# Optimization experiments

Hardware: AMD Instinct MI355X
Metric: run time of the kernel (lower is better)

## Reference

```python
import jax, jax.numpy as jnp
import numpy as np

N = 20000        # nodes
E = 320000       # edges (avg degree 16)
F_IN = 128       # node_features
F2 = 64          # second_features (per-head out dim, LSTM hidden)
H = 8            # heads
D1 = H * F2      # 512, concat output of GATConv / LSTM input
NEG_SLOPE = 0.2  # GATConv default leaky_relu slope


def _gat_conv(x, src, dst, W, att_src, att_dst, bias):
    """PyG GATConv (concat=True, self-loops added, eval-mode dropout)."""
    n = x.shape[0]
    h = (x @ W).reshape(n, H, -1)                      # [N,H,F]
    a_s = (h * att_src).sum(-1)                        # [N,H]
    a_d = (h * att_dst).sum(-1)                        # [N,H]
    e = jax.nn.leaky_relu(a_s[src] + a_d[dst], NEG_SLOPE)   # [E',H]
    m = jax.ops.segment_max(e, dst, num_segments=n)    # [N,H]
    m = jnp.where(jnp.isfinite(m), m, 0.0)
    ex = jnp.exp(e - m[dst])
    denom = jax.ops.segment_sum(ex, dst, num_segments=n)
    alpha = ex / (denom[dst] + 1e-16)                  # [E',H]
    msg = h[src] * alpha[:, :, None]                   # [E',H,F]
    out = jax.ops.segment_sum(msg, dst, num_segments=n)  # [N,H,F]
    return out.reshape(n, -1) + bias                   # [N,H*F]


def _lstm_step(x, W_ih, W_hh, b_ih, b_hh):
    """Single-timestep PyTorch LSTM with zero initial (h0, c0). x: [N,D1]."""
    h0 = jnp.zeros((x.shape[0], F2), x.dtype)
    gates = x @ W_ih.T + b_ih + h0 @ W_hh.T + b_hh     # [N,4*F2]
    i, f, g, o = jnp.split(gates, 4, axis=-1)
    c = jax.nn.sigmoid(f) * 0.0 + jax.nn.sigmoid(i) * jnp.tanh(g)
    h = jax.nn.sigmoid(o) * jnp.tanh(c)
    return h, (h, c)


def setup_inputs() -> dict:
    key = jax.random.key(0)
    ks = jax.random.split(key, 16)

    def glorot(k, shape, fan_in):
        return jax.random.normal(k, shape, jnp.float32) * (1.0 / np.sqrt(fan_in))

    return {
        "x": jax.random.normal(ks[0], (N, F_IN), jnp.float32),
        "edge_index": jax.random.randint(ks[1], (2, E), 0, N, jnp.int32),
        "edge_weight": jax.random.uniform(ks[2], (E,), jnp.float32),
        # GATConv 1: F_IN -> H*F2
        "W1": glorot(ks[3], (F_IN, H * F2), F_IN),
        "att_src1": glorot(ks[4], (H, F2), F2),
        "att_dst1": glorot(ks[5], (H, F2), F2),
        "bias1": jnp.zeros((H * F2,), jnp.float32),
        # LSTM: input D1 -> hidden F2
        "W_ih": glorot(ks[6], (4 * F2, D1), D1),
        "W_hh": glorot(ks[7], (4 * F2, F2), F2),
        "b_ih": jnp.zeros((4 * F2,), jnp.float32),
        "b_hh": jnp.zeros((4 * F2,), jnp.float32),
        # GATConv 2: F2 -> H*F2
        "W2": glorot(ks[8], (F2, H * F2), F2),
        "att_src2": glorot(ks[9], (H, F2), F2),
        "att_dst2": glorot(ks[10], (H, F2), F2),
        "bias2": jnp.zeros((H * F2,), jnp.float32),
    }


def reference(x, edge_index, edge_weight, W1, att_src1, att_dst1, bias1,
              W_ih, W_hh, b_ih, b_hh, W2, att_src2, att_dst2, bias2):
    # edge_weight is accepted but unused, matching the original forward.
    loops = jnp.arange(N, dtype=edge_index.dtype)
    src = jnp.concatenate([edge_index[0], loops])      # add self-loops (PyG default)
    dst = jnp.concatenate([edge_index[1], loops])

    h = _gat_conv(x, src, dst, W1, att_src1, att_dst1, bias1)   # [N,512]
    h, hidden2 = _lstm_step(h, W_ih, W_hh, b_ih, b_hh)          # [N,64]
    h = jax.nn.relu(h)
    h = _gat_conv(h, src, dst, W2, att_src2, att_dst2, bias2)   # [N,512]
    return jax.nn.softmax(h, axis=1)
```

## Files before the change

### kernel.cpp

```cpp
#include <hip/hip_runtime.h>
#include <math.h>


__global__ void count_kernel(const int* __restrict__ dst, int* __restrict__ deg, int E) {
  int i = blockIdx.x * 256 + threadIdx.x;
  if (i < E) atomicAdd(&deg[dst[i]], 1);
}

__global__ void scan_kernel(const int* __restrict__ deg, int* __restrict__ rowptr, int n) {
  __shared__ int buf[1024];
  const int tid = threadIdx.x;
  const int i0 = tid * 20;
  int v[20];
  int tsum = 0;
#pragma unroll
  for (int k = 0; k < 20; ++k) {
    int i = i0 + k;
    v[k] = (i < n) ? (deg[i] + 1) : 0;
    tsum += v[k];
  }
  int incl = tsum;
  buf[tid] = incl;
  __syncthreads();
  for (int s = 1; s < 1024; s <<= 1) {
    int t = (tid >= (unsigned)s) ? buf[tid - s] : 0;
    __syncthreads();
    incl += t;
    buf[tid] = incl;
    __syncthreads();
  }
  int excl = incl - tsum;
#pragma unroll
  for (int k = 0; k < 20; ++k) {
    int i = i0 + k;
    if (i < n) rowptr[i] = excl;
    excl += v[k];
  }
  if (tid == 1023) rowptr[n] = incl;
}

__global__ void scatter_kernel(const int* __restrict__ src, const int* __restrict__ dst,
                               const int* __restrict__ rowptr, int* __restrict__ wp,
                               int* __restrict__ col, int E, int n) {
  int i = blockIdx.x * 256 + threadIdx.x;
  if (i < E) {
    int d = dst[i];
    int p = rowptr[d] + atomicAdd(&wp[d], 1);
    col[p] = src[i];
  } else if (i < E + n) {
    int d = i - E;
    int p = rowptr[d] + atomicAdd(&wp[d], 1);
    col[p] = d;
  }
}


template <int BMt, int BNt, int TNt>
__global__ __launch_bounds__(256) void gemm_kernel(
    const float* __restrict__ A, const float* __restrict__ B,
    float* __restrict__ C, const float* __restrict__ bias,
    int M, int K, int lda, int ldb, int ldc,
    int aZ, int bZ, int cZ, int biasZ) {
  constexpr int BKt = 16;
  constexpr int TM = BMt / 16;
  constexpr int AST = (BMt * BKt) / 1024;
  constexpr int BST = (BKt * BNt) / 1024;
  static_assert(BNt == 16 * TNt, "layout");
  __shared__ float As[2][BKt][BMt + 4];
  __shared__ float Bs[2][BKt][BNt];
  const int z = blockIdx.z;
  A += (size_t)z * aZ;
  B += (size_t)z * bZ;
  C += (size_t)z * cZ;
  const int tid = threadIdx.x;
  const int bm = blockIdx.y * BMt;
  const int bn = blockIdx.x * BNt;
  const int tm = (tid >> 4) * TM;
  const int tn = (tid & 15) * TNt;
  int arow_[AST], akq_[AST];
#pragma unroll
  for (int i = 0; i < AST; ++i) {
    int idx = tid + i * 256;
    arow_[i] = idx >> 2;
    akq_[i] = (idx & 3) * 4;
  }
  int bkr_[BST], bc4_[BST];
#pragma unroll
  for (int i = 0; i < BST; ++i) {
    int idx = tid + i * 256;
    bkr_[i] = idx / (BNt / 4);
    bc4_[i] = (idx % (BNt / 4)) * 4;
  }
  float4 pa[AST], pb[BST];
#pragma unroll
  for (int i = 0; i < AST; ++i) {
    pa[i] = make_float4(0.f, 0.f, 0.f, 0.f);
    if (bm + arow_[i] < M)
      pa[i] = *reinterpret_cast<const float4*>(A + (size_t)(bm + arow_[i]) * lda + akq_[i]);
  }
#pragma unroll
  for (int i = 0; i < BST; ++i)
    pb[i] = *reinterpret_cast<const float4*>(B + (size_t)bkr_[i] * ldb + bn + bc4_[i]);
#pragma unroll
  for (int i = 0; i < AST; ++i) {
    As[0][akq_[i] + 0][arow_[i]] = pa[i].x; As[0][akq_[i] + 1][arow_[i]] = pa[i].y;
    As[0][akq_[i] + 2][arow_[i]] = pa[i].z; As[0][akq_[i] + 3][arow_[i]] = pa[i].w;
  }
#pragma unroll
  for (int i = 0; i < BST; ++i)
    *reinterpret_cast<float4*>(&Bs[0][bkr_[i]][bc4_[i]]) = pb[i];
  __syncthreads();
  float acc[TM][TNt] = {};
  int buf = 0;
  for (int k0 = 0; k0 < K; k0 += BKt) {
    const int kn = k0 + BKt;
    if (kn < K) {
#pragma unroll
      for (int i = 0; i < AST; ++i) {
        float4 t = make_float4(0.f, 0.f, 0.f, 0.f);
        if (bm + arow_[i] < M)
          t = *reinterpret_cast<const float4*>(A + (size_t)(bm + arow_[i]) * lda + kn + akq_[i]);
        pa[i] = t;
      }
#pragma unroll
      for (int i = 0; i < BST; ++i)
        pb[i] = *reinterpret_cast<const float4*>(B + (size_t)(kn + bkr_[i]) * ldb + bn + bc4_[i]);
    }
#pragma unroll
    for (int k = 0; k < BKt; ++k) {
      float a[TM], b[TNt];
#pragma unroll
      for (int i = 0; i < TM; ++i) a[i] = As[buf][k][tm + i];
#pragma unroll
      for (int q = 0; q < TNt / 4; ++q) {
        float4 bv = *reinterpret_cast<const float4*>(&Bs[buf][k][tn + q * 4]);
        b[q * 4 + 0] = bv.x; b[q * 4 + 1] = bv.y;
        b[q * 4 + 2] = bv.z; b[q * 4 + 3] = bv.w;
      }
#pragma unroll
      for (int i = 0; i < TM; ++i)
#pragma unroll
        for (int j = 0; j < TNt; ++j) acc[i][j] = fmaf(a[i], b[j], acc[i][j]);
    }
    if (kn < K) {
      int nb = buf ^ 1;
#pragma unroll
      for (int i = 0; i < AST; ++i) {
        As[nb][akq_[i] + 0][arow_[i]] = pa[i].x; As[nb][akq_[i] + 1][arow_[i]] = pa[i].y;
        As[nb][akq_[i] + 2][arow_[i]] = pa[i].z; As[nb][akq_[i] + 3][arow_[i]] = pa[i].w;
      }
#pragma unroll
      for (int i = 0; i < BST; ++i)
        *reinterpret_cast<float4*>(&Bs[nb][bkr_[i]][bc4_[i]]) = pb[i];
      __syncthreads();
      buf = nb;
    }
  }
  float bz[TNt];
#pragma unroll
  for (int j = 0; j < TNt; ++j) bz[j] = 0.f;
  if (bias) {
#pragma unroll
    for (int q = 0; q < TNt / 4; ++q) {
      float4 bv = *reinterpret_cast<const float4*>(bias + (size_t)z * biasZ + bn + tn + q * 4);
      bz[q * 4 + 0] = bv.x; bz[q * 4 + 1] = bv.y;
      bz[q * 4 + 2] = bv.z; bz[q * 4 + 3] = bv.w;
    }
  }
#pragma unroll
  for (int i = 0; i < TM; ++i) {
    int m = bm + tm + i;
    if (m < M) {
#pragma unroll
      for (int q = 0; q < TNt / 4; ++q) {
        float4 o;
        o.x = acc[i][q * 4 + 0] + bz[q * 4 + 0];
        o.y = acc[i][q * 4 + 1] + bz[q * 4 + 1];
        o.z = acc[i][q * 4 + 2] + bz[q * 4 + 2];
        o.w = acc[i][q * 4 + 3] + bz[q * 4 + 3];
        *reinterpret_cast<float4*>(C + (size_t)m * ldc + bn + tn + q * 4) = o;
      }
    }
  }
}


__global__ void prep_all_kernel(const float* __restrict__ W_ih, const float* __restrict__ b_ih,
                                const float* __restrict__ b_hh, const float* __restrict__ W1,
                                const float* __restrict__ as1, const float* __restrict__ ad1,
                                const float* __restrict__ W2, const float* __restrict__ as2,
                                const float* __restrict__ ad2,
                                int* __restrict__ degwp, float* __restrict__ Wt,
                                float* __restrict__ bsum, float* __restrict__ watt1,
                                float* __restrict__ watt2, int n2) {
  int idx = blockIdx.x * 256 + threadIdx.x;
  if (idx < n2) {
    degwp[idx] = 0;
    return;
  }
  int t = idx - n2;
  if (t < 98304) {
    int k = t / 192, jp = t - k * 192;
    int j = (jp < 64) ? jp : jp + 64;
    Wt[t] = W_ih[(size_t)j * 512 + k];
    return;
  }
  t -= 98304;
  if (t < 192) {
    int j = (t < 64) ? t : t + 64;
    bsum[t] = b_ih[j] + b_hh[j];
    return;
  }
  t -= 192;
  if (t < 2048) {
    int f = t >> 4, c = t & 15;
    int k = c & 7;
    const float* att = ((c < 8) ? as1 : ad1) + k * 64;
    const float* w = W1 + (size_t)f * 512 + k * 64;
    float s = 0.f;
#pragma unroll
    for (int j = 0; j < 64; ++j) s = fmaf(w[j], att[j], s);
    watt1[t] = s;
    return;
  }
  t -= 2048;
  if (t < 1024) {
    int f = t >> 4, c = t & 15;
    int k = c & 7;
    const float* att = ((c < 8) ? as2 : ad2) + k * 64;
    const float* w = W2 + (size_t)f * 512 + k * 64;
    float s = 0.f;
#pragma unroll
    for (int j = 0; j < 64; ++j) s = fmaf(w[j], att[j], s);
    watt2[t] = s;
  }
}


template <int F>
__global__ __launch_bounds__(256) void attcoef_kernel(
    const float* __restrict__ feat, const float* __restrict__ watt,
    float* __restrict__ a_s, float* __restrict__ a_d, int n) {
  __shared__ float rows[16 * F];
  __shared__ float wbuf[F * 16];
  const int n0 = blockIdx.x * 16;
  const int tid = threadIdx.x;
  if (n0 + 16 <= n) {
    const float4* g = reinterpret_cast<const float4*>(feat + (size_t)n0 * F);
    float4* l = reinterpret_cast<float4*>(rows);
    for (int i = tid; i < 16 * F / 4; i += 256) l[i] = g[i];
  } else {
    for (int i = tid; i < 16 * F; i += 256) {
      int r = i / F;
      rows[i] = (n0 + r < n) ? feat[(size_t)(n0 + r) * F + (i - r * F)] : 0.f;
    }
  }
  {
    const float4* g = reinterpret_cast<const float4*>(watt);
    float4* l = reinterpret_cast<float4*>(wbuf);
    for (int i = tid; i < F * 16 / 4; i += 256) l[i] = g[i];
  }
  __syncthreads();
  const int local = tid >> 4, c = tid & 15;
  float s = 0.f;
#pragma unroll 8
  for (int f = 0; f < F; ++f) s = fmaf(rows[local * F + f], wbuf[f * 16 + c], s);
  const int node = n0 + local;
  if (node < n) {
    if (c < 8) a_s[(size_t)node * 8 + c] = s;
    else       a_d[(size_t)node * 8 + (c - 8)] = s;
  }
}


template <int F>
__global__ __launch_bounds__(256) void gat_aggregate_wave(
    const float* __restrict__ feat, const float* __restrict__ a_s,
    const float* __restrict__ a_d, const int* __restrict__ rowptr,
    const int* __restrict__ col, float* __restrict__ agg, int n) {
  constexpr int F4 = F / 4;
  constexpr int HPG = (F == 128) ? 4 : 2;
  __shared__ float s_alpha[4][8][8];
  __shared__ int s_cols[4][8];
  const int wid = threadIdx.x >> 6;
  const int lane = threadIdx.x & 63;
  const int node = blockIdx.x * 4 + wid;
  if (node >= n) return;
  const int start = rowptr[node];
  const int deg = rowptr[node + 1] - start;
  const int j = lane >> 3;
  const int h = lane & 7;
  const float adh = a_d[(size_t)node * 8 + h];
  float den = 0.f;
  for (int e = j; e < deg; e += 8) {
    int s = col[start + e];
    float v = a_s[(size_t)s * 8 + h] + adh;
    v = (v > 0.f) ? v : 0.2f * v;
    den += __expf(v);
  }
  den += __shfl_xor(den, 8);
  den += __shfl_xor(den, 16);
  den += __shfl_xor(den, 32);
  const float inv = 1.f / (den + 1e-16f);
  const int f4 = lane & (F4 - 1);
  const int hbase = (lane / F4) * HPG;
  float4 acc0 = make_float4(0.f, 0.f, 0.f, 0.f);
  float4 acc1 = make_float4(0.f, 0.f, 0.f, 0.f);
  float4 acc2 = make_float4(0.f, 0.f, 0.f, 0.f);
  float4 acc3 = make_float4(0.f, 0.f, 0.f, 0.f);
  for (int c0 = 0; c0 < deg; c0 += 8) {
    float aval = 0.f;
    int sj = 0;
    if (c0 + j < deg) {
      sj = col[start + c0 + j];
      float v = a_s[(size_t)sj * 8 + h] + adh;
      v = (v > 0.f) ? v : 0.2f * v;
      aval = __expf(v) * inv;
    }
    s_alpha[wid][j][h] = aval;
    if (h == 0) s_cols[wid][j] = sj;
    __builtin_amdgcn_wave_barrier();
    const int ce = min(8, deg - c0);
    for (int e = 0; e < ce; ++e) {
      int s = s_cols[wid][e];
      float4 fv = *reinterpret_cast<const float4*>(feat + (size_t)s * F + f4 * 4);
      if constexpr (HPG == 4) {
        float4 al = *reinterpret_cast<const float4*>(&s_alpha[wid][e][hbase]);
        acc0.x = fmaf(al.x, fv.x, acc0.x); acc0.y = fmaf(al.x, fv.y, acc0.y);
        acc0.z = fmaf(al.x, fv.z, acc0.z); acc0.w = fmaf(al.x, fv.w, acc0.w);
        acc1.x = fmaf(al.y, fv.x, acc1.x); acc1.y = fmaf(al.y, fv.y, acc1.y);
        acc1.z = fmaf(al.y, fv.z, acc1.z); acc1.w = fmaf(al.y, fv.w, acc1.w);
        acc2.x = fmaf(al.z, fv.x, acc2.x); acc2.y = fmaf(al.z, fv.y, acc2.y);
        acc2.z = fmaf(al.z, fv.z, acc2.z); acc2.w = fmaf(al.z, fv.w, acc2.w);
        acc3.x = fmaf(al.w, fv.x, acc3.x); acc3.y = fmaf(al.w, fv.y, acc3.y);
        acc3.z = fmaf(al.w, fv.z, acc3.z); acc3.w = fmaf(al.w, fv.w, acc3.w);
      } else {
        float2 al = *reinterpret_cast<const float2*>(&s_alpha[wid][e][hbase]);
        acc0.x = fmaf(al.x, fv.x, acc0.x); acc0.y = fmaf(al.x, fv.y, acc0.y);
        acc0.z = fmaf(al.x, fv.z, acc0.z); acc0.w = fmaf(al.x, fv.w, acc0.w);
        acc1.x = fmaf(al.y, fv.x, acc1.x); acc1.y = fmaf(al.y, fv.y, acc1.y);
        acc1.z = fmaf(al.y, fv.z, acc1.z); acc1.w = fmaf(al.y, fv.w, acc1.w);
      }
    }
    __builtin_amdgcn_wave_barrier();
  }
  float* outp = agg + (size_t)node * 8 * F + (size_t)hbase * F + f4 * 4;
  *reinterpret_cast<float4*>(outp) = acc0;
  *reinterpret_cast<float4*>(outp + F) = acc1;
  if constexpr (HPG == 4) {
    *reinterpret_cast<float4*>(outp + 2 * F) = acc2;
    *reinterpret_cast<float4*>(outp + 3 * F) = acc3;
  }
}


__global__ __launch_bounds__(256) void lstm_act_attcoef_kernel(
    const float* __restrict__ gp0, const float* __restrict__ bsum,
    const float* __restrict__ watt2, float* __restrict__ h2,
    float* __restrict__ a_s2, float* __restrict__ a_d2, int n) {
  __shared__ float h2t[4][64];
  __shared__ float wbuf[64 * 16];
  const int tid = threadIdx.x;
  reinterpret_cast<float4*>(wbuf)[tid] = reinterpret_cast<const float4*>(watt2)[tid];
  const int nl = tid >> 6, j = tid & 63;
  const int node = blockIdx.x * 4 + nl;
  float hv = 0.f;
  if (node < n) {
    const float* g0 = gp0 + (size_t)node * 192;
    const float* g1 = g0 + (size_t)n * 192;
    float iv = g0[j] + g1[j] + bsum[j];
    float gv = g0[64 + j] + g1[64 + j] + bsum[64 + j];
    float ov = g0[128 + j] + g1[128 + j] + bsum[128 + j];
    float c = (1.f / (1.f + __expf(-iv))) * tanhf(gv);
    hv = fmaxf((1.f / (1.f + __expf(-ov))) * tanhf(c), 0.f);
    h2[(size_t)node * 64 + j] = hv;
  }
  h2t[nl][j] = hv;
  __syncthreads();
  if (j < 16 && node < n) {
    float s = 0.f;
#pragma unroll 16
    for (int f = 0; f < 64; ++f) s = fmaf(h2t[nl][f], wbuf[f * 16 + j], s);
    if (j < 8) a_s2[(size_t)node * 8 + j] = s;
    else       a_d2[(size_t)node * 8 + (j - 8)] = s;
  }
}


__global__ __launch_bounds__(256) void softmax512_wave(const float* __restrict__ in,
                                                       float* __restrict__ out, int n) {
  const int wid = threadIdx.x >> 6, lane = threadIdx.x & 63;
  const int node = blockIdx.x * 4 + wid;
  if (node >= n) return;
  const float4* ip = reinterpret_cast<const float4*>(in + (size_t)node * 512);
  float4 v0 = ip[lane];
  float4 v1 = ip[64 + lane];
  float m = fmaxf(fmaxf(fmaxf(v0.x, v0.y), fmaxf(v0.z, v0.w)),
                  fmaxf(fmaxf(v1.x, v1.y), fmaxf(v1.z, v1.w)));
#pragma unroll
  for (int d = 1; d < 64; d <<= 1) m = fmaxf(m, __shfl_xor(m, d));
  float4 e0, e1;
  e0.x = __expf(v0.x - m); e0.y = __expf(v0.y - m);
  e0.z = __expf(v0.z - m); e0.w = __expf(v0.w - m);
  e1.x = __expf(v1.x - m); e1.y = __expf(v1.y - m);
  e1.z = __expf(v1.z - m); e1.w = __expf(v1.w - m);
  float s = e0.x + e0.y + e0.z + e0.w + e1.x + e1.y + e1.z + e1.w;
#pragma unroll
  for (int d = 1; d < 64; d <<= 1) s += __shfl_xor(s, d);
  float inv = 1.f / s;
  e0.x *= inv; e0.y *= inv; e0.z *= inv; e0.w *= inv;
  e1.x *= inv; e1.y *= inv; e1.z *= inv; e1.w *= inv;
  float4* op = reinterpret_cast<float4*>(out + (size_t)node * 512);
  op[lane] = e0;
  op[64 + lane] = e1;
}


extern "C" void kernel_launch(void* const* d_in, const int* in_sizes, int n_in,
                              void* d_out, int out_size, void* d_ws, size_t ws_size,
                              hipStream_t stream) {
  const float* x      = (const float*)d_in[0];
  const int*   ei     = (const int*)d_in[1];
  const float* W1     = (const float*)d_in[3];
  const float* att_s1 = (const float*)d_in[4];
  const float* att_d1 = (const float*)d_in[5];
  const float* bias1  = (const float*)d_in[6];
  const float* W_ih   = (const float*)d_in[7];
  const float* b_ih   = (const float*)d_in[9];
  const float* b_hh   = (const float*)d_in[10];
  const float* W2     = (const float*)d_in[11];
  const float* att_s2 = (const float*)d_in[12];
  const float* att_d2 = (const float*)d_in[13];
  const float* bias2  = (const float*)d_in[14];
  float* out = (float*)d_out;

  const int N = in_sizes[0] / 128;
  const int E = in_sizes[1] / 2;
  const int* src = ei;
  const int* dst = ei + E;

  char* p = (char*)d_ws;
  auto alloc = [&](size_t bytes) {
    char* r = p;
    p += (bytes + 255) & ~(size_t)255;
    return r;
  };
  float* slotA = (float*)alloc((size_t)N * 1024 * 4);
  float* slotB = (float*)alloc((size_t)N * 512 * 4);
  float* a_s1 = (float*)alloc((size_t)N * 8 * 4);
  float* a_d1 = (float*)alloc((size_t)N * 8 * 4);
  float* a_s2 = (float*)alloc((size_t)N * 8 * 4);
  float* a_d2 = (float*)alloc((size_t)N * 8 * 4);
  float* watt1 = (float*)alloc(128 * 16 * 4);
  float* watt2 = (float*)alloc(64 * 16 * 4);
  float* Wt   = (float*)alloc((size_t)512 * 192 * 4);
  float* bsum = (float*)alloc(192 * 4);
  int* deg    = (int*)alloc((size_t)2 * N * 4);
  int* wp     = deg + N;
  int* rowptr = (int*)alloc((size_t)(N + 1) * 4);
  int* col    = (int*)alloc((size_t)(E + N) * 4);

  float* agg1   = slotA;
  float* g1     = slotB;
  float* gates2 = slotA;
  float* h2     = slotA + (size_t)N * 384;
  float* agg2   = slotA + (size_t)N * 448;
  float* h3p    = slotB;

  {
    int total = 2 * N + 98304 + 192 + 2048 + 1024;
    prep_all_kernel<<<(total + 255) / 256, 256, 0, stream>>>(
        W_ih, b_ih, b_hh, W1, att_s1, att_d1, W2, att_s2, att_d2,
        deg, Wt, bsum, watt1, watt2, 2 * N);
  }

  count_kernel<<<(E + 255) / 256, 256, 0, stream>>>(dst, deg, E);
  scan_kernel<<<1, 1024, 0, stream>>>(deg, rowptr, N);
  scatter_kernel<<<(E + N + 255) / 256, 256, 0, stream>>>(src, dst, rowptr, wp, col, E, N);

  attcoef_kernel<128><<<(N + 15) / 16, 256, 0, stream>>>(x, watt1, a_s1, a_d1, N);
  gat_aggregate_wave<128><<<(N + 3) / 4, 256, 0, stream>>>(x, a_s1, a_d1, rowptr, col, agg1, N);
  {
    dim3 g(1, (N + 127) / 128, 8);
    gemm_kernel<128, 64, 4><<<g, 256, 0, stream>>>(agg1, W1, g1, bias1,
                                                   N, 128, 1024, 512, 512, 128, 64, 64, 64);
  }

  {
    dim3 g(3, (N + 63) / 64, 2);
    gemm_kernel<64, 64, 4><<<g, 256, 0, stream>>>(g1, Wt, gates2, nullptr,
                                                  N, 256, 512, 192, 192,
                                                  256, 256 * 192, N * 192, 0);
  }
  lstm_act_attcoef_kernel<<<(N + 3) / 4, 256, 0, stream>>>(gates2, bsum, watt2,
                                                           h2, a_s2, a_d2, N);

  gat_aggregate_wave<64><<<(N + 3) / 4, 256, 0, stream>>>(h2, a_s2, a_d2, rowptr, col, agg2, N);
  {
    dim3 g(1, (N + 127) / 128, 8);
    gemm_kernel<128, 64, 4><<<g, 256, 0, stream>>>(agg2, W2, h3p, bias2,
                                                   N, 64, 512, 512, 512, 64, 64, 64, 64);
  }
  softmax512_wave<<<(N + 3) / 4, 256, 0, stream>>>(h3p, out, N);
}
```

Before: 374.8 us.

## Replace FP32 SIMT GEMMs with split-bf16 MFMA GEMM using three-product emulation

Replaces the scalar FMA tiled GEMM with an MFMA kernel that splits each fp32 operand into high and low bf16 parts and accumulates three bf16 products, which approximates fp32 accuracy. Weight matrices are pre-split and transposed into bf16 pairs in the prep kernel. The LSTM gate GEMM is also turned from a split-K over two halves into a single K=512 pass, so the gate add in the activation kernel is dropped. The aim is to move GEMM work onto the matrix cores. The cost is per-tile conversion of A to bf16 inside the kernel, scalar output stores, and a single-buffered LDS pipeline.

```diff
diff --git a/kernel.cpp b/kernel.cpp
--- a/kernel.cpp
+++ b/kernel.cpp
@@ -1,5 +1,6 @@
 #include <hip/hip_runtime.h>
 #include <math.h>
+#include <stdint.h>
 
 
 __global__ void count_kernel(const int* __restrict__ dst, int* __restrict__ deg, int E) {
@@ -55,130 +56,116 @@
 }
 
 
-template <int BMt, int BNt, int TNt>
-__global__ __launch_bounds__(256) void gemm_kernel(
-    const float* __restrict__ A, const float* __restrict__ B,
-    float* __restrict__ C, const float* __restrict__ bias,
-    int M, int K, int lda, int ldb, int ldc,
-    int aZ, int bZ, int cZ, int biasZ) {
-  constexpr int BKt = 16;
-  constexpr int TM = BMt / 16;
-  constexpr int AST = (BMt * BKt) / 1024;
-  constexpr int BST = (BKt * BNt) / 1024;
-  static_assert(BNt == 16 * TNt, "layout");
-  __shared__ float As[2][BKt][BMt + 4];
-  __shared__ float Bs[2][BKt][BNt];
+__device__ __forceinline__ uint16_t bf16r(float x) {
+  uint32_t u = __float_as_uint(x);
+  return (uint16_t)((u + 0x7FFFu + ((u >> 16) & 1u)) >> 16);
+}
+__device__ __forceinline__ void bfsplit(float x, uint16_t& h, uint16_t& l) {
+  h = bf16r(x);
+  float hf = __uint_as_float((uint32_t)h << 16);
+  l = bf16r(x - hf);
+}
+
+using bf16x8 = __attribute__((ext_vector_type(8))) short;
+using f32x4  = __attribute__((ext_vector_type(4))) float;
+
+
+__global__ __launch_bounds__(256) void gemm_mfma(
+    const float* __restrict__ A, const uint16_t* __restrict__ Bh,
+    const uint16_t* __restrict__ Bl, float* __restrict__ C,
+    const float* __restrict__ bias,
+    int M, int K, int lda, int aZ, int bZ, int ldc, int cZ, int biasZ) {
+  constexpr int BM = 128, BN = 64, BK = 64;
+  __shared__ __align__(16) uint16_t sAh[BM * BK], sAl[BM * BK];
+  __shared__ __align__(16) uint16_t sBh[BN * BK], sBl[BN * BK];
   const int z = blockIdx.z;
   A += (size_t)z * aZ;
-  B += (size_t)z * bZ;
+  Bh += (size_t)z * bZ;
+  Bl += (size_t)z * bZ;
   C += (size_t)z * cZ;
   const int tid = threadIdx.x;
-  const int bm = blockIdx.y * BMt;
-  const int bn = blockIdx.x * BNt;
-  const int tm = (tid >> 4) * TM;
-  const int tn = (tid & 15) * TNt;
-  int arow_[AST], akq_[AST];
-#pragma unroll
-  for (int i = 0; i < AST; ++i) {
-    int idx = tid + i * 256;
-    arow_[i] = idx >> 2;
-    akq_[i] = (idx & 3) * 4;
-  }
-  int bkr_[BST], bc4_[BST];
-#pragma unroll
-  for (int i = 0; i < BST; ++i) {
-    int idx = tid + i * 256;
-    bkr_[i] = idx / (BNt / 4);
-    bc4_[i] = (idx % (BNt / 4)) * 4;
-  }
-  float4 pa[AST], pb[BST];
-#pragma unroll
-  for (int i = 0; i < AST; ++i) {
-    pa[i] = make_float4(0.f, 0.f, 0.f, 0.f);
-    if (bm + arow_[i] < M)
-      pa[i] = *reinterpret_cast<const float4*>(A + (size_t)(bm + arow_[i]) * lda + akq_[i]);
-  }
-#pragma unroll
-  for (int i = 0; i < BST; ++i)
-    pb[i] = *reinterpret_cast<const float4*>(B + (size_t)bkr_[i] * ldb + bn + bc4_[i]);
-#pragma unroll
-  for (int i = 0; i < AST; ++i) {
-    As[0][akq_[i] + 0][arow_[i]] = pa[i].x; As[0][akq_[i] + 1][arow_[i]] = pa[i].y;
-    As[0][akq_[i] + 2][arow_[i]] = pa[i].z; As[0][akq_[i] + 3][arow_[i]] = pa[i].w;
-  }
-#pragma unroll
-  for (int i = 0; i < BST; ++i)
-    *reinterpret_cast<float4*>(&Bs[0][bkr_[i]][bc4_[i]]) = pb[i];
-  __syncthreads();
-  float acc[TM][TNt] = {};
-  int buf = 0;
-  for (int k0 = 0; k0 < K; k0 += BKt) {
-    const int kn = k0 + BKt;
-    if (kn < K) {
-#pragma unroll
-      for (int i = 0; i < AST; ++i) {
-        float4 t = make_float4(0.f, 0.f, 0.f, 0.f);
-        if (bm + arow_[i] < M)
-          t = *reinterpret_cast<const float4*>(A + (size_t)(bm + arow_[i]) * lda + kn + akq_[i]);
-        pa[i] = t;
+  const int wid = tid >> 6, lane = tid & 63;
+  const int bm = blockIdx.y * BM;
+  const int bn = blockIdx.x * BN;
+  const int fr = lane & 15;
+  const int kg = lane >> 4;
+  const int mbase = wid * 32;
+  f32x4 acc[2][4] = {};
+
+  for (int k0 = 0; k0 < K; k0 += BK) {
+#pragma unroll
+    for (int s = 0; s < 8; ++s) {
+      int idx = tid + s * 256;
+      int row = idx >> 4;
+      int c4 = (idx & 15) * 4;
+      float4 v = make_float4(0.f, 0.f, 0.f, 0.f);
+      if (bm + row < M)
+        v = *reinterpret_cast<const float4*>(A + (size_t)(bm + row) * lda + k0 + c4);
+      ushort4 h, l;
+      bfsplit(v.x, h.x, l.x); bfsplit(v.y, h.y, l.y);
+      bfsplit(v.z, h.z, l.z); bfsplit(v.w, h.w, l.w);
+      int off = (row * BK + c4) * 2;
+      off ^= (row & 7) << 4;
+      *reinterpret_cast<ushort4*>(reinterpret_cast<char*>(sAh) + off) = h;
+      *reinterpret_cast<ushort4*>(reinterpret_cast<char*>(sAl) + off) = l;
+    }
+#pragma unroll
+    for (int s = 0; s < 2; ++s) {
+      int idx = tid + s * 256;
+      int row = idx >> 3;
+      int c8 = (idx & 7) * 8;
+      uint4 vh = *reinterpret_cast<const uint4*>(Bh + (size_t)(bn + row) * K + k0 + c8);
+      uint4 vl = *reinterpret_cast<const uint4*>(Bl + (size_t)(bn + row) * K + k0 + c8);
+      int off = (row * BK + c8) * 2;
+      off ^= (row & 7) << 4;
+      *reinterpret_cast<uint4*>(reinterpret_cast<char*>(sBh) + off) = vh;
+      *reinterpret_cast<uint4*>(reinterpret_cast<char*>(sBl) + off) = vl;
+    }
+    __syncthreads();
+#pragma unroll
+    for (int ks = 0; ks < 2; ++ks) {
+      bf16x8 ah[2], al[2], bh[4], bl[4];
+#pragma unroll
+      for (int i = 0; i < 2; ++i) {
+        int m = mbase + i * 16 + fr;
+        int off = m * (BK * 2) + ks * 64 + kg * 16;
+        off ^= (m & 7) << 4;
+        ah[i] = *reinterpret_cast<const bf16x8*>(reinterpret_cast<const char*>(sAh) + off);
+        al[i] = *reinterpret_cast<const bf16x8*>(reinterpret_cast<const char*>(sAl) + off);
       }
 #pragma unroll
-      for (int i = 0; i < BST; ++i)
-        pb[i] = *reinterpret_cast<const float4*>(B + (size_t)(kn + bkr_[i]) * ldb + bn + bc4_[i]);
-    }
-#pragma unroll
-    for (int k = 0; k < BKt; ++k) {
-      float a[TM], b[TNt];
-#pragma unroll
-      for (int i = 0; i < TM; ++i) a[i] = As[buf][k][tm + i];
-#pragma unroll
-      for (int q = 0; q < TNt / 4; ++q) {
-        float4 bv = *reinterpret_cast<const float4*>(&Bs[buf][k][tn + q * 4]);
-        b[q * 4 + 0] = bv.x; b[q * 4 + 1] = bv.y;
-        b[q * 4 + 2] = bv.z; b[q * 4 + 3] = bv.w;
+      for (int j = 0; j < 4; ++j) {
+        int n = j * 16 + fr;
+        int off = n * (BK * 2) + ks * 64 + kg * 16;
+        off ^= (n & 7) << 4;
+        bh[j] = *reinterpret_cast<const bf16x8*>(reinterpret_cast<const char*>(sBh) + off);
+        bl[j] = *reinterpret_cast<const bf16x8*>(reinterpret_cast<const char*>(sBl) + off);
       }
 #pragma unroll
-      for (int i = 0; i < TM; ++i)
-#pragma unroll
-        for (int j = 0; j < TNt; ++j) acc[i][j] = fmaf(a[i], b[j], acc[i][j]);
-    }
-    if (kn < K) {
-      int nb = buf ^ 1;
-#pragma unroll
-      for (int i = 0; i < AST; ++i) {
-        As[nb][akq_[i] + 0][arow_[i]] = pa[i].x; As[nb][akq_[i] + 1][arow_[i]] = pa[i].y;
-        As[nb][akq_[i] + 2][arow_[i]] = pa[i].z; As[nb][akq_[i] + 3][arow_[i]] = pa[i].w;
-      }
-#pragma unroll
-      for (int i = 0; i < BST; ++i)
-        *reinterpret_cast<float4*>(&Bs[nb][bkr_[i]][bc4_[i]]) = pb[i];
-      __syncthreads();
-      buf = nb;
-    }
-  }
-  float bz[TNt];
-#pragma unroll
-  for (int j = 0; j < TNt; ++j) bz[j] = 0.f;
-  if (bias) {
-#pragma unroll
-    for (int q = 0; q < TNt / 4; ++q) {
-      float4 bv = *reinterpret_cast<const float4*>(bias + (size_t)z * biasZ + bn + tn + q * 4);
-      bz[q * 4 + 0] = bv.x; bz[q * 4 + 1] = bv.y;
-      bz[q * 4 + 2] = bv.z; bz[q * 4 + 3] = bv.w;
-    }
-  }
-#pragma unroll
-  for (int i = 0; i < TM; ++i) {
-    int m = bm + tm + i;
-    if (m < M) {
-#pragma unroll
-      for (int q = 0; q < TNt / 4; ++q) {
-        float4 o;
-        o.x = acc[i][q * 4 + 0] + bz[q * 4 + 0];
-        o.y = acc[i][q * 4 + 1] + bz[q * 4 + 1];
-        o.z = acc[i][q * 4 + 2] + bz[q * 4 + 2];
-        o.w = acc[i][q * 4 + 3] + bz[q * 4 + 3];
-        *reinterpret_cast<float4*>(C + (size_t)m * ldc + bn + tn + q * 4) = o;
+      for (int i = 0; i < 2; ++i)
+#pragma unroll
+        for (int j = 0; j < 4; ++j) {
+          acc[i][j] = __builtin_amdgcn_mfma_f32_16x16x32_bf16(ah[i], bh[j], acc[i][j], 0, 0, 0);
+          acc[i][j] = __builtin_amdgcn_mfma_f32_16x16x32_bf16(al[i], bh[j], acc[i][j], 0, 0, 0);
+          acc[i][j] = __builtin_amdgcn_mfma_f32_16x16x32_bf16(ah[i], bl[j], acc[i][j], 0, 0, 0);
+        }
+    }
+    __syncthreads();
+  }
+  float bz[4];
+#pragma unroll
+  for (int j = 0; j < 4; ++j)
+    bz[j] = bias ? bias[(size_t)z * biasZ + bn + j * 16 + fr] : 0.f;
+#pragma unroll
+  for (int i = 0; i < 2; ++i) {
+    int mr = bm + mbase + i * 16 + kg * 4;
+#pragma unroll
+    for (int r = 0; r < 4; ++r) {
+      int m = mr + r;
+      if (m < M) {
+#pragma unroll
+        for (int j = 0; j < 4; ++j)
+          C[(size_t)m * ldc + bn + j * 16 + fr] = acc[i][j][r] + bz[j];
       }
     }
   }
@@ -190,7 +177,10 @@
                                 const float* __restrict__ as1, const float* __restrict__ ad1,
                                 const float* __restrict__ W2, const float* __restrict__ as2,
                                 const float* __restrict__ ad2,
-                                int* __restrict__ degwp, float* __restrict__ Wt,
+                                int* __restrict__ degwp,
+                                uint16_t* __restrict__ Wtbh, uint16_t* __restrict__ Wtbl,
+                                uint16_t* __restrict__ Bt1h, uint16_t* __restrict__ Bt1l,
+                                uint16_t* __restrict__ Bt2h, uint16_t* __restrict__ Bt2l,
                                 float* __restrict__ bsum, float* __restrict__ watt1,
                                 float* __restrict__ watt2, int n2) {
   int idx = blockIdx.x * 256 + threadIdx.x;
@@ -200,12 +190,30 @@
   }
   int t = idx - n2;
   if (t < 98304) {
-    int k = t / 192, jp = t - k * 192;
+    int jp = t >> 9, k = t & 511;
     int j = (jp < 64) ? jp : jp + 64;
-    Wt[t] = W_ih[(size_t)j * 512 + k];
+    uint16_t h, l;
+    bfsplit(W_ih[(size_t)j * 512 + k], h, l);
+    Wtbh[t] = h; Wtbl[t] = l;
     return;
   }
   t -= 98304;
+  if (t < 65536) {
+    int n = t >> 7, k = t & 127;
+    uint16_t h, l;
+    bfsplit(W1[(size_t)k * 512 + n], h, l);
+    Bt1h[t] = h; Bt1l[t] = l;
+    return;
+  }
+  t -= 65536;
+  if (t < 32768) {
+    int n = t >> 6, k = t & 63;
+    uint16_t h, l;
+    bfsplit(W2[(size_t)k * 512 + n], h, l);
+    Bt2h[t] = h; Bt2l[t] = l;
+    return;
+  }
+  t -= 32768;
   if (t < 192) {
     int j = (t < 64) ? t : t + 64;
     bsum[t] = b_ih[j] + b_hh[j];
@@ -355,7 +363,7 @@
 
 
 __global__ __launch_bounds__(256) void lstm_act_attcoef_kernel(
-    const float* __restrict__ gp0, const float* __restrict__ bsum,
+    const float* __restrict__ gates, const float* __restrict__ bsum,
     const float* __restrict__ watt2, float* __restrict__ h2,
     float* __restrict__ a_s2, float* __restrict__ a_d2, int n) {
   __shared__ float h2t[4][64];
@@ -366,11 +374,10 @@
   const int node = blockIdx.x * 4 + nl;
   float hv = 0.f;
   if (node < n) {
-    const float* g0 = gp0 + (size_t)node * 192;
-    const float* g1 = g0 + (size_t)n * 192;
-    float iv = g0[j] + g1[j] + bsum[j];
-    float gv = g0[64 + j] + g1[64 + j] + bsum[64 + j];
-    float ov = g0[128 + j] + g1[128 + j] + bsum[128 + j];
+    const float* g0 = gates + (size_t)node * 192;
+    float iv = g0[j] + bsum[j];
+    float gv = g0[64 + j] + bsum[64 + j];
+    float ov = g0[128 + j] + bsum[128 + j];
     float c = (1.f / (1.f + __expf(-iv))) * tanhf(gv);
     hv = fmaxf((1.f / (1.f + __expf(-ov))) * tanhf(c), 0.f);
     h2[(size_t)node * 64 + j] = hv;
@@ -453,7 +460,12 @@
   float* a_d2 = (float*)alloc((size_t)N * 8 * 4);
   float* watt1 = (float*)alloc(128 * 16 * 4);
   float* watt2 = (float*)alloc(64 * 16 * 4);
-  float* Wt   = (float*)alloc((size_t)512 * 192 * 4);
+  uint16_t* Wtbh = (uint16_t*)alloc((size_t)192 * 512 * 2);
+  uint16_t* Wtbl = (uint16_t*)alloc((size_t)192 * 512 * 2);
+  uint16_t* Bt1h = (uint16_t*)alloc((size_t)512 * 128 * 2);
+  uint16_t* Bt1l = (uint16_t*)alloc((size_t)512 * 128 * 2);
+  uint16_t* Bt2h = (uint16_t*)alloc((size_t)512 * 64 * 2);
+  uint16_t* Bt2l = (uint16_t*)alloc((size_t)512 * 64 * 2);
   float* bsum = (float*)alloc(192 * 4);
   int* deg    = (int*)alloc((size_t)2 * N * 4);
   int* wp     = deg + N;
@@ -468,10 +480,10 @@
   float* h3p    = slotB;
 
   {
-    int total = 2 * N + 98304 + 192 + 2048 + 1024;
+    int total = 2 * N + 98304 + 65536 + 32768 + 192 + 2048 + 1024;
     prep_all_kernel<<<(total + 255) / 256, 256, 0, stream>>>(
         W_ih, b_ih, b_hh, W1, att_s1, att_d1, W2, att_s2, att_d2,
-        deg, Wt, bsum, watt1, watt2, 2 * N);
+        deg, Wtbh, Wtbl, Bt1h, Bt1l, Bt2h, Bt2l, bsum, watt1, watt2, 2 * N);
   }
 
   count_kernel<<<(E + 255) / 256, 256, 0, stream>>>(dst, deg, E);
@@ -482,15 +494,15 @@
   gat_aggregate_wave<128><<<(N + 3) / 4, 256, 0, stream>>>(x, a_s1, a_d1, rowptr, col, agg1, N);
   {
     dim3 g(1, (N + 127) / 128, 8);
-    gemm_kernel<128, 64, 4><<<g, 256, 0, stream>>>(agg1, W1, g1, bias1,
-                                                   N, 128, 1024, 512, 512, 128, 64, 64, 64);
+    gemm_mfma<<<g, 256, 0, stream>>>(agg1, Bt1h, Bt1l, g1, bias1,
+                                     N, 128, 1024, 128, 64 * 128,
+                                     512, 64, 64);
   }
 
   {
-    dim3 g(3, (N + 63) / 64, 2);
-    gemm_kernel<64, 64, 4><<<g, 256, 0, stream>>>(g1, Wt, gates2, nullptr,
-                                                  N, 256, 512, 192, 192,
-                                                  256, 256 * 192, N * 192, 0);
+    dim3 g(3, (N + 127) / 128, 1);
+    gemm_mfma<<<g, 256, 0, stream>>>(g1, Wtbh, Wtbl, gates2, nullptr,
+                                     N, 512, 512, 0, 0, 192, 0, 0);
   }
   lstm_act_attcoef_kernel<<<(N + 3) / 4, 256, 0, stream>>>(gates2, bsum, watt2,
                                                            h2, a_s2, a_d2, N);
@@ -498,8 +510,9 @@
   gat_aggregate_wave<64><<<(N + 3) / 4, 256, 0, stream>>>(h2, a_s2, a_d2, rowptr, col, agg2, N);
   {
     dim3 g(1, (N + 127) / 128, 8);
-    gemm_kernel<128, 64, 4><<<g, 256, 0, stream>>>(agg2, W2, h3p, bias2,
-                                                   N, 64, 512, 512, 512, 64, 64, 64, 64);
+    gemm_mfma<<<g, 256, 0, stream>>>(agg2, Bt2h, Bt2l, h3p, bias2,
+                                     N, 64, 512, 64, 64 * 64,
+                                     512, 64, 64);
   }
   softmax512_wave<<<(N + 3) / 4, 256, 0, stream>>>(h3p, out, N);
 }
```

New measurement: 338.2 us. 1.11x faster.
